# Kernel optimization log

Hardware: AMD Instinct MI355X
Metric: run time of the kernel (lower is better)

The kernel has to match this reference:

```python
import jax, jax.numpy as jnp
import numpy as np

H = 128
W = 128
DELTA = 7000.0  # sigmainv in the original (delta default 7000)


def setup_inputs() -> dict:
    key = jax.random.key(0)
    k1, k2, k3, k4 = jax.random.split(key, 4)
    B, P, F, TH, TW = 2, 300, 512, 512, 512
    points_bxpx3 = jax.random.uniform(k1, (B, P, 3), jnp.float32) * 2.0 - 1.0  # NDC cube [-1,1]
    faces_fx3 = jax.random.randint(k2, (F, 3), 0, P, dtype=jnp.int32)
    uv_bxpx2 = jax.random.uniform(k3, (B, P, 2), jnp.float32)  # texcoords in [0,1]
    texture_bx3xthxtw = jax.random.uniform(k4, (B, 3, TH, TW), jnp.float32)
    return {"points_bxpx3": points_bxpx3, "faces_fx3": faces_fx3,
            "uv_bxpx2": uv_bxpx2, "texture_bx3xthxtw": texture_bx3xthxtw}


def _edge(ax, ay, bx, by, px, py):
    # signed area * 2 of triangle (a, b, p); standard edge function
    return (bx - ax) * (py - ay) - (by - ay) * (px - ax)


def _seg_d2(ax, ay, bx, by, px, py):
    # squared distance from point p to segment (a, b)
    abx, aby = bx - ax, by - ay
    apx, apy = px - ax, py - ay
    denom = abx * abx + aby * aby + 1e-12
    t = jnp.clip((apx * abx + apy * aby) / denom, 0.0, 1.0)
    dx = apx - t * abx
    dy = apy - t * aby
    return dx * dx + dy * dy


def _rasterize(points_bxpx3, faces_fx3, feats_bxfx3xd, height, width, delta):
    """Soft DIB-R-style rasterizer.
    Returns (imfeat [B,H,W,D], improb [B,H,W,1]).
    """
    B = points_bxpx3.shape[0]
    v = points_bxpx3[:, faces_fx3]                      # (B,F,3,3) gathered face vertices
    x0, x1, x2 = (v[:, :, i, 0][:, :, None, None] for i in range(3))
    y0, y1, y2 = (v[:, :, i, 1][:, :, None, None] for i in range(3))
    z0, z1, z2 = (v[:, :, i, 2][:, :, None, None] for i in range(3))

    # pixel-center grid in NDC; y flipped (top row = +1)
    px = ((jnp.arange(width, dtype=points_bxpx3.dtype) + 0.5) / width * 2.0 - 1.0)[None, None, None, :]
    py = (1.0 - (jnp.arange(height, dtype=points_bxpx3.dtype) + 0.5) / height * 2.0)[None, None, :, None]

    area = _edge(x0, y0, x1, y1, x2, y2)                # (B,F,1,1) == normal_z (cross-product z)
    front = area > 1e-8                                  # front-facing (normalz > 0) cull
    inv_area = 1.0 / jnp.where(front, area, 1.0)

    w0 = _edge(x1, y1, x2, y2, px, py) * inv_area        # (B,F,H,W) barycentrics
    w1 = _edge(x2, y2, x0, y0, px, py) * inv_area
    w2 = _edge(x0, y0, x1, y1, px, py) * inv_area
    inside = front & (w0 >= 0) & (w1 >= 0) & (w2 >= 0)

    z_pix = w0 * z0 + w1 * z1 + w2 * z2                  # interpolated depth
    zbuf = jnp.where(inside, z_pix, -1e9)
    best = jnp.argmax(zbuf, axis=1)                      # (B,H,W) nearest covering face
    hit = jnp.any(inside, axis=1)[..., None].astype(points_bxpx3.dtype)  # (B,H,W,1)

    # gather winning barycentrics and per-face vertex features
    w = jnp.stack([w0, w1, w2], axis=-1)                 # (B,F,H,W,3)
    idx = jnp.broadcast_to(best[:, None, :, :, None], (B, 1, height, width, 3))
    wb = jnp.take_along_axis(w, idx, axis=1)[:, 0]       # (B,H,W,3)
    fb = jax.vmap(lambda f, i: f[i])(feats_bxfx3xd, best)  # (B,H,W,3,D)
    imfeat = jnp.einsum('bhwk,bhwkd->bhwd', wb, fb) * hit

    # soft coverage: prob of each face = exp(-delta * d2(pixel, triangle)); z-buffer blend
    d2 = jnp.minimum(
        jnp.minimum(_seg_d2(x0, y0, x1, y1, px, py), _seg_d2(x1, y1, x2, y2, px, py)),
        _seg_d2(x2, y2, x0, y0, px, py))
    d2 = jnp.where(inside, 0.0, d2)
    p = jnp.where(front, jnp.exp(-delta * d2), 0.0)      # (B,F,H,W)
    log_miss = jnp.sum(jnp.log1p(-jnp.clip(p, 0.0, 1.0 - 1e-7)), axis=1)  # (B,H,W)
    improb = (1.0 - jnp.exp(log_miss))[..., None]
    return imfeat, improb


def _fragmentshader(imtexcoords, texture_bx3xthxtw, hardmask):
    # bilinear texture sampling; background is zero
    B, C, TH, TW = texture_bx3xthxtw.shape
    u = jnp.clip(imtexcoords[..., 0], 0.0, 1.0)
    vv = jnp.clip(imtexcoords[..., 1], 0.0, 1.0)
    fx = u * (TW - 1)
    fy = (1.0 - vv) * (TH - 1)
    x0 = jnp.floor(fx).astype(jnp.int32); x1 = jnp.minimum(x0 + 1, TW - 1)
    y0 = jnp.floor(fy).astype(jnp.int32); y1 = jnp.minimum(y0 + 1, TH - 1)
    wx = (fx - x0)[:, None]; wy = (fy - y0)[:, None]     # (B,1,H,W)

    def g(tex, yy, xx):  # tex (C,TH,TW), yy/xx (H,W) -> (C,H,W)
        return tex[:, yy, xx]
    c00 = jax.vmap(g)(texture_bx3xthxtw, y0, x0)
    c01 = jax.vmap(g)(texture_bx3xthxtw, y0, x1)
    c10 = jax.vmap(g)(texture_bx3xthxtw, y1, x0)
    c11 = jax.vmap(g)(texture_bx3xthxtw, y1, x1)
    col = (c00 * (1 - wx) * (1 - wy) + c01 * wx * (1 - wy)
           + c10 * (1 - wx) * wy + c11 * wx * wy)        # (B,C,H,W)
    return col.transpose(0, 2, 3, 1) * hardmask          # (B,H,W,C)


def reference(points_bxpx3, faces_fx3, uv_bxpx2, texture_bx3xthxtw):
    # texture mode: per-face vertex features = [u, v, mask=1]
    uvf = uv_bxpx2[:, faces_fx3]                          # (B,F,3,2)
    ones = jnp.ones_like(uvf[..., :1])
    feats = jnp.concatenate([uvf, ones], axis=-1)         # (B,F,3,3)
    imfeat, improb = _rasterize(points_bxpx3, faces_fx3, feats, H, W, DELTA)
    imtexcoords = imfeat[..., :2]
    hardmask = jax.lax.stop_gradient(imfeat[..., 2:3])    # .detach() in the original
    imrender = _fragmentshader(imtexcoords, texture_bx3xthxtw, hardmask)
    return imrender, improb
```

## Files before the change

### kernel.cpp

```cpp
#include <hip/hip_runtime.h>
#include <math.h>

constexpr int kB = 2, kP = 300, kF = 512, kH = 128, kW = 128, kTH = 512, kTW = 512;
constexpr float kDelta = 7000.0f;
constexpr float kCut = 0.0363f;
constexpr float kThr2 = 0.012928f;
constexpr float kIntThr = 0.0785f;
constexpr float kLogInside = -15.9423847f;

__device__ __forceinline__ unsigned zmap(float f) {
    unsigned b = __float_as_uint(f);
    return (b & 0x80000000u) ? ~b : (b | 0x80000000u);
}

__global__ __launch_bounds__(512, 4) void render_all(const float* __restrict__ pts,
                                                     const int* __restrict__ faces,
                                                     const float* __restrict__ uvs,
                                                     const float* __restrict__ tex,
                                                     float* __restrict__ out) {
    __shared__ float4 sF[8][kF];
    __shared__ unsigned long long s_best[64];
    __shared__ float s_lm[64];
    __shared__ int s_wsum[8];
    float4* s_pxW = sF[0];
    int4* s_pxO = (int4*)(sF[0] + 64);

    int tile = (int)blockIdx.x;
    int b = tile >> 8;
    int rem = tile & 255;
    int ty = rem >> 4, tx = rem & 15;
    int tid = (int)threadIdx.x;
    int lane = tid & 63;
    int wv = tid >> 6;

    {
        int f = tid;
        int i0 = faces[f * 3 + 0], i1 = faces[f * 3 + 1], i2 = faces[f * 3 + 2];
        const float* pb = pts + b * kP * 3;
        float x0 = pb[i0 * 3], y0 = pb[i0 * 3 + 1], z0 = pb[i0 * 3 + 2];
        float x1 = pb[i1 * 3], y1 = pb[i1 * 3 + 1], z1 = pb[i1 * 3 + 2];
        float x2 = pb[i2 * 3], y2 = pb[i2 * 3 + 1], z2 = pb[i2 * 3 + 2];
        const float* ub = uvs + b * (kP * 2);
        float u0 = ub[i0 * 2], vv0 = ub[i0 * 2 + 1];
        float u1 = ub[i1 * 2], vv1 = ub[i1 * 2 + 1];
        float u2 = ub[i2 * 2], vv2 = ub[i2 * 2 + 1];
        float area = (x1 - x0) * (y2 - y0) - (y1 - y0) * (x2 - x0);
        bool front = area > 1e-8f;

        if (tid < 64) { s_best[tid] = 0ull; s_lm[tid] = 0.0f; }
        sF[0][f] = make_float4(0.0f, 0.0f, -1e30f, 0.0f);
        sF[1][f] = make_float4(0.0f, -1e30f, 0.0f, 0.0f);
        sF[2][f] = make_float4(-1e30f, 0.0f, 0.0f, 0.0f);
        unsigned long long bal = __ballot(front);
        if (lane == 0) s_wsum[wv] = __popcll(bal);
        __syncthreads();

        int base = 0;
#pragma unroll
        for (int w = 0; w < 8; ++w) base += (w < wv) ? s_wsum[w] : 0;
        int k = base + __popcll(bal & ((1ull << lane) - 1ull));

        if (front) {
            int slot = ((k & 7) << 6) | (k >> 3);
            float inv_a = 1.0f / area;
            float e0x = x2 - x1, e0y = y2 - y1;
            float e1x = x0 - x2, e1y = y0 - y2;
            float e2x = x1 - x0, e2y = y1 - y0;
            float l0 = fmaf(e0x, e0x, e0y * e0y);
            float l1 = fmaf(e1x, e1x, e1y * e1y);
            float l2 = fmaf(e2x, e2x, e2y * e2y);
            float s0 = rsqrtf(l0 + 1e-12f);
            float s1 = rsqrtf(l1 + 1e-12f);
            float s2 = rsqrtf(l2 + 1e-12f);
            float A0 = -e0y * s0, B0 = e0x * s0, C0 = (e0y * x1 - e0x * y1) * s0;
            float A1 = -e1y * s1, B1 = e1x * s1, C1 = (e1y * x2 - e1x * y2) * s1;
            float A2 = -e2y * s2, B2 = e2x * s2, C2 = (e2y * x0 - e2x * y0) * s2;
            float a0 = -e0y * inv_a, b0 = e0x * inv_a, c0 = (e0y * x1 - e0x * y1) * inv_a;
            float a1 = -e1y * inv_a, b1 = e1x * inv_a, c1 = (e1y * x2 - e1x * y2) * inv_a;
            float a2 = -e2y * inv_a, b2 = e2x * inv_a, c2 = (e2y * x0 - e2x * y0) * inv_a;
            sF[0][slot] = make_float4(A0, B0, C0, A1);
            sF[1][slot] = make_float4(B1, C1, A2, B2);
            sF[2][slot] = make_float4(C2,
                                      a0 * z0 + a1 * z1 + a2 * z2,
                                      b0 * z0 + b1 * z1 + b2 * z2,
                                      c0 * z0 + c1 * z1 + c2 * z2);
            sF[3][slot] = make_float4(e0x * s0, e0y * s0,
                                      -(e0x * x1 + e0y * y1) * s0, l0 * s0);
            sF[4][slot] = make_float4(e1x * s1, e1y * s1,
                                      -(e1x * x2 + e1y * y2) * s1, l1 * s1);
            sF[5][slot] = make_float4(e2x * s2, e2y * s2,
                                      -(e2x * x0 + e2y * y0) * s2, l2 * s2);
            sF[6][slot] = make_float4(a0 * u0 + a1 * u1 + a2 * u2,
                                      b0 * u0 + b1 * u1 + b2 * u2,
                                      c0 * u0 + c1 * u1 + c2 * u2, 0.0f);
            sF[7][slot] = make_float4(a0 * vv0 + a1 * vv1 + a2 * vv2,
                                      b0 * vv0 + b1 * vv1 + b2 * vv2,
                                      c0 * vv0 + c1 * vv1 + c2 * vv2, 0.0f);
        }
    }
    __syncthreads();

    int pyi = ty * 8 + (lane >> 3);
    int pxi = tx * 8 + (lane & 7);
    float px = ((float)pxi + 0.5f) * (2.0f / 128.0f) - 1.0f;
    float py = 1.0f - ((float)pyi + 0.5f) * (2.0f / 128.0f);

    float cx = (float)(tx * 8 + 4) * (2.0f / 128.0f) - 1.0f;
    float cy = 1.0f - (float)(ty * 8 + 4) * (2.0f / 128.0f);
    unsigned long long me, mi;
    {
        int slt = (wv << 6) + lane;
        float4 a4 = sF[0][slt];
        float4 b4 = sF[1][slt];
        float4 c4 = sF[2][slt];
        float4 t0 = sF[3][slt];
        float4 t1 = sF[4][slt];
        float4 t2 = sF[5][slt];
        float L0 = fmaf(a4.x, cx, fmaf(a4.y, cy, a4.z));
        float L1 = fmaf(a4.w, cx, fmaf(b4.x, cy, b4.y));
        float L2 = fmaf(b4.z, cx, fmaf(b4.w, cy, c4.x));
        float minc = fminf(fminf(L0, L1), L2);
        float s0 = fmaf(t0.x, cx, fmaf(t0.y, cy, t0.z));
        float s1 = fmaf(t1.x, cx, fmaf(t1.y, cy, t1.z));
        float s2 = fmaf(t2.x, cx, fmaf(t2.y, cy, t2.z));
        float q0 = L0 * L0, q1 = L1 * L1, q2 = L2 * L2;
        float c0 = (s0 >= 0.0f && s0 <= t0.w) ? q0 : 1e30f;
        float c1 = (s1 >= 0.0f && s1 <= t1.w) ? q1 : 1e30f;
        float c2 = (s2 >= 0.0f && s2 <= t2.w) ? q2 : 1e30f;
        float dv1 = fmaf(s0, s0, q0);
        float dv2 = fmaf(s1, s1, q1);
        float dv0 = fmaf(s2, s2, q2);
        float d2c = fminf(fminf(fminf(c0, c1), fminf(c2, dv0)), fminf(dv1, dv2));
        bool inter = minc >= kIntThr;
        bool admit = (minc >= 0.0f) | (d2c <= kThr2);
        mi = __ballot(inter);
        me = __ballot(admit && !inter);
    }

    float bestz = -1e9f;
    int besti = 1 << 30, icnt = 0;
    float lm = 0.0f;

    icnt += (int)__popcll(mi);
    while (mi) {
        int l = (int)__builtin_ctzll(mi);
        mi &= (mi - 1);
        int fs = (wv << 6) + l;
        int k = (l << 3) | wv;
        float4 h2 = sF[2][fs];
        float z = fmaf(h2.y, px, fmaf(h2.z, py, h2.w));
        if (z > bestz || (z == bestz && k < besti)) { bestz = z; besti = k; }
    }

    while (me) {
        int l = (int)__builtin_ctzll(me);
        me &= (me - 1);
        int fs = (wv << 6) + l;
        int k = (l << 3) | wv;
        float4 h0 = sF[0][fs];
        float4 h1 = sF[1][fs];
        float4 h2 = sF[2][fs];
        float4 t0 = sF[3][fs];
        float4 t1 = sF[4][fs];
        float4 t2 = sF[5][fs];
        float L0 = fmaf(h0.x, px, fmaf(h0.y, py, h0.z));
        float L1 = fmaf(h0.w, px, fmaf(h1.x, py, h1.y));
        float L2 = fmaf(h1.z, px, fmaf(h1.w, py, h2.x));
        float minL = fminf(fminf(L0, L1), L2);
        bool inside = minL >= 0.0f;
        float z = fmaf(h2.y, px, fmaf(h2.z, py, h2.w));
        if (inside && (z > bestz || (z == bestz && k < besti))) { bestz = z; besti = k; }
        icnt += inside ? 1 : 0;
        float s0 = fmaf(t0.x, px, fmaf(t0.y, py, t0.z));
        float s1 = fmaf(t1.x, px, fmaf(t1.y, py, t1.z));
        float s2 = fmaf(t2.x, px, fmaf(t2.y, py, t2.z));
        float q0 = L0 * L0, q1 = L1 * L1, q2 = L2 * L2;
        float c0 = (s0 >= 0.0f && s0 <= t0.w) ? q0 : 1e30f;
        float c1 = (s1 >= 0.0f && s1 <= t1.w) ? q1 : 1e30f;
        float c2 = (s2 >= 0.0f && s2 <= t2.w) ? q2 : 1e30f;
        float dv1 = fmaf(s0, s0, q0);
        float dv2 = fmaf(s1, s1, q1);
        float dv0 = fmaf(s2, s2, q2);
        float d2 = fminf(fminf(fminf(c0, c1), fminf(c2, dv0)), fminf(dv1, dv2));
        bool need = (!inside) & (fminf(fminf(fabsf(L0), fabsf(L1)), fabsf(L2)) < kCut);
        d2 = need ? d2 : 30.0f;
        float p = __expf(-kDelta * d2);
        p = fminf(p, 1.0f - 1e-7f);
        lm += __logf(1.0f - p);
    }
    lm = fmaf((float)icnt, kLogInside, lm);

    if (besti < (1 << 30)) {
        unsigned long long key = ((unsigned long long)zmap(bestz) << 32) |
                                 (unsigned long long)(511 - besti);
        atomicMax(&s_best[lane], key);
    }
    atomicAdd(&s_lm[lane], lm);
    __syncthreads();

    if (tid < 64) {
        unsigned long long key = s_best[tid];
        float improb = 1.0f - expf(s_lm[tid]);
        float u = 0.0f, v = 0.0f, mk = 0.0f;
        if (key != 0ull) {
            int bi = 511 - (int)(key & 0xFFFFFFFFull);
            int slot = ((bi & 7) << 6) | (bi >> 3);
            float4 uq = sF[6][slot];
            float4 vq = sF[7][slot];
            u = fmaf(uq.x, px, fmaf(uq.y, py, uq.z));
            v = fmaf(vq.x, px, fmaf(vq.y, py, vq.z));
            mk = 1.0f;
        }
        float uc = fminf(fmaxf(u, 0.0f), 1.0f);
        float vc = fminf(fmaxf(v, 0.0f), 1.0f);
        float fx = uc * (float)(kTW - 1);
        float fy = (1.0f - vc) * (float)(kTH - 1);
        int xi0 = (int)floorf(fx), yi0 = (int)floorf(fy);
        int xi1 = min(xi0 + 1, kTW - 1), yi1 = min(yi0 + 1, kTH - 1);
        float wx = fx - (float)xi0, wy = fy - (float)yi0;
        float w00 = (1.0f - wx) * (1.0f - wy) * mk;
        float w01 = wx * (1.0f - wy) * mk;
        float w10 = (1.0f - wx) * wy * mk;
        float w11 = wx * wy * mk;
        s_pxW[tid] = make_float4(w00, w01, w10, w11);
        s_pxO[tid] = make_int4(yi0 * kTW + xi0, yi0 * kTW + xi1,
                               yi1 * kTW + xi0, yi1 * kTW + xi1);
        out[kB * kH * kW * 3 + (b * kH + pyi) * kW + pxi] = improb;
    }
    __syncthreads();

    if (tid < 192) {
        int pix = tid & 63;
        int c = tid >> 6;
        float4 w = s_pxW[pix];
        int4 o = s_pxO[pix];
        const float* tc = tex + ((size_t)b * 3 + c) * kTH * kTW;
        float col = tc[o.x] * w.x + tc[o.y] * w.y + tc[o.z] * w.z + tc[o.w] * w.w;
        int qy = ty * 8 + (pix >> 3);
        int qx = tx * 8 + (pix & 7);
        out[((b * kH + qy) * kW + qx) * 3 + c] = col;
    }
}

extern "C" void kernel_launch(void* const* d_in, const int* in_sizes, int n_in,
                              void* d_out, int out_size, void* d_ws, size_t ws_size,
                              hipStream_t stream) {
    const float* pts = (const float*)d_in[0];
    const int* faces = (const int*)d_in[1];
    const float* uvs = (const float*)d_in[2];
    const float* tex = (const float*)d_in[3];
    float* out = (float*)d_out;
    render_all<<<kB * 256, 512, 0, stream>>>(pts, faces, uvs, tex, out);
}
```

Measured before the change: 17.26 us.

## Drop front-face compaction prefix sum and unroll face loops by two

Face setup no longer compacts front-facing faces through a ballot prefix sum and an extra block barrier. Each face now goes to a fixed slot, and back faces get sentinel edge values so they fail every test. The intersection and edge-candidate loops now handle two faces per iteration, so their shared-memory loads can be issued together for more instruction-level parallelism. The cost is more register pressure and a duplicate evaluation when the count is odd, which is masked by the 'two' flag. Because faces are no longer compacted, back faces can sit in slots that the later per-wave scan may still visit.

Result: slower. 17.62 us (+2.1%).

```diff
diff --git a/kernel.cpp b/kernel.cpp
--- a/kernel.cpp
+++ b/kernel.cpp
@@ -21,7 +21,6 @@
     __shared__ float4 sF[8][kF];
     __shared__ unsigned long long s_best[64];
     __shared__ float s_lm[64];
-    __shared__ int s_wsum[8];
     float4* s_pxW = sF[0];
     int4* s_pxO = (int4*)(sF[0] + 64);
 
@@ -48,55 +47,48 @@
         bool front = area > 1e-8f;
 
         if (tid < 64) { s_best[tid] = 0ull; s_lm[tid] = 0.0f; }
-        sF[0][f] = make_float4(0.0f, 0.0f, -1e30f, 0.0f);
-        sF[1][f] = make_float4(0.0f, -1e30f, 0.0f, 0.0f);
-        sF[2][f] = make_float4(-1e30f, 0.0f, 0.0f, 0.0f);
-        unsigned long long bal = __ballot(front);
-        if (lane == 0) s_wsum[wv] = __popcll(bal);
-        __syncthreads();
-
-        int base = 0;
-#pragma unroll
-        for (int w = 0; w < 8; ++w) base += (w < wv) ? s_wsum[w] : 0;
-        int k = base + __popcll(bal & ((1ull << lane) - 1ull));
-
+
+        int slot = ((f & 7) << 6) | (f >> 3);
+        float inv_a = front ? (1.0f / area) : 0.0f;
+        float e0x = x2 - x1, e0y = y2 - y1;
+        float e1x = x0 - x2, e1y = y0 - y2;
+        float e2x = x1 - x0, e2y = y1 - y0;
+        float l0 = fmaf(e0x, e0x, e0y * e0y);
+        float l1 = fmaf(e1x, e1x, e1y * e1y);
+        float l2 = fmaf(e2x, e2x, e2y * e2y);
+        float s0 = rsqrtf(l0 + 1e-12f);
+        float s1 = rsqrtf(l1 + 1e-12f);
+        float s2 = rsqrtf(l2 + 1e-12f);
+        float A0 = -e0y * s0, B0 = e0x * s0, C0 = (e0y * x1 - e0x * y1) * s0;
+        float A1 = -e1y * s1, B1 = e1x * s1, C1 = (e1y * x2 - e1x * y2) * s1;
+        float A2 = -e2y * s2, B2 = e2x * s2, C2 = (e2y * x0 - e2x * y0) * s2;
+        float a0 = -e0y * inv_a, b0 = e0x * inv_a, c0 = (e0y * x1 - e0x * y1) * inv_a;
+        float a1 = -e1y * inv_a, b1 = e1x * inv_a, c1 = (e1y * x2 - e1x * y2) * inv_a;
+        float a2 = -e2y * inv_a, b2 = e2x * inv_a, c2 = (e2y * x0 - e2x * y0) * inv_a;
         if (front) {
-            int slot = ((k & 7) << 6) | (k >> 3);
-            float inv_a = 1.0f / area;
-            float e0x = x2 - x1, e0y = y2 - y1;
-            float e1x = x0 - x2, e1y = y0 - y2;
-            float e2x = x1 - x0, e2y = y1 - y0;
-            float l0 = fmaf(e0x, e0x, e0y * e0y);
-            float l1 = fmaf(e1x, e1x, e1y * e1y);
-            float l2 = fmaf(e2x, e2x, e2y * e2y);
-            float s0 = rsqrtf(l0 + 1e-12f);
-            float s1 = rsqrtf(l1 + 1e-12f);
-            float s2 = rsqrtf(l2 + 1e-12f);
-            float A0 = -e0y * s0, B0 = e0x * s0, C0 = (e0y * x1 - e0x * y1) * s0;
-            float A1 = -e1y * s1, B1 = e1x * s1, C1 = (e1y * x2 - e1x * y2) * s1;
-            float A2 = -e2y * s2, B2 = e2x * s2, C2 = (e2y * x0 - e2x * y0) * s2;
-            float a0 = -e0y * inv_a, b0 = e0x * inv_a, c0 = (e0y * x1 - e0x * y1) * inv_a;
-            float a1 = -e1y * inv_a, b1 = e1x * inv_a, c1 = (e1y * x2 - e1x * y2) * inv_a;
-            float a2 = -e2y * inv_a, b2 = e2x * inv_a, c2 = (e2y * x0 - e2x * y0) * inv_a;
             sF[0][slot] = make_float4(A0, B0, C0, A1);
             sF[1][slot] = make_float4(B1, C1, A2, B2);
             sF[2][slot] = make_float4(C2,
                                       a0 * z0 + a1 * z1 + a2 * z2,
                                       b0 * z0 + b1 * z1 + b2 * z2,
                                       c0 * z0 + c1 * z1 + c2 * z2);
-            sF[3][slot] = make_float4(e0x * s0, e0y * s0,
-                                      -(e0x * x1 + e0y * y1) * s0, l0 * s0);
-            sF[4][slot] = make_float4(e1x * s1, e1y * s1,
-                                      -(e1x * x2 + e1y * y2) * s1, l1 * s1);
-            sF[5][slot] = make_float4(e2x * s2, e2y * s2,
-                                      -(e2x * x0 + e2y * y0) * s2, l2 * s2);
-            sF[6][slot] = make_float4(a0 * u0 + a1 * u1 + a2 * u2,
-                                      b0 * u0 + b1 * u1 + b2 * u2,
-                                      c0 * u0 + c1 * u1 + c2 * u2, 0.0f);
-            sF[7][slot] = make_float4(a0 * vv0 + a1 * vv1 + a2 * vv2,
-                                      b0 * vv0 + b1 * vv1 + b2 * vv2,
-                                      c0 * vv0 + c1 * vv1 + c2 * vv2, 0.0f);
-        }
+        } else {
+            sF[0][slot] = make_float4(0.0f, 0.0f, -1e30f, 0.0f);
+            sF[1][slot] = make_float4(0.0f, -1e30f, 0.0f, 0.0f);
+            sF[2][slot] = make_float4(-1e30f, 0.0f, 0.0f, 0.0f);
+        }
+        sF[3][slot] = make_float4(e0x * s0, e0y * s0,
+                                  -(e0x * x1 + e0y * y1) * s0, l0 * s0);
+        sF[4][slot] = make_float4(e1x * s1, e1y * s1,
+                                  -(e1x * x2 + e1y * y2) * s1, l1 * s1);
+        sF[5][slot] = make_float4(e2x * s2, e2y * s2,
+                                  -(e2x * x0 + e2y * y0) * s2, l2 * s2);
+        sF[6][slot] = make_float4(a0 * u0 + a1 * u1 + a2 * u2,
+                                  b0 * u0 + b1 * u1 + b2 * u2,
+                                  c0 * u0 + c1 * u1 + c2 * u2, 0.0f);
+        sF[7][slot] = make_float4(a0 * vv0 + a1 * vv1 + a2 * vv2,
+                                  b0 * vv0 + b1 * vv1 + b2 * vv2,
+                                  c0 * vv0 + c1 * vv1 + c2 * vv2, 0.0f);
     }
     __syncthreads();
 
@@ -145,48 +137,77 @@
     while (mi) {
         int l = (int)__builtin_ctzll(mi);
         mi &= (mi - 1);
-        int fs = (wv << 6) + l;
-        int k = (l << 3) | wv;
-        float4 h2 = sF[2][fs];
-        float z = fmaf(h2.y, px, fmaf(h2.z, py, h2.w));
-        if (z > bestz || (z == bestz && k < besti)) { bestz = z; besti = k; }
+        bool two = mi != 0;
+        int l2 = two ? (int)__builtin_ctzll(mi) : l;
+        if (two) mi &= (mi - 1);
+        float4 hA = sF[2][(wv << 6) + l];
+        float4 hB = sF[2][(wv << 6) + l2];
+        int kA = (l << 3) | wv, kB = (l2 << 3) | wv;
+        float zA = fmaf(hA.y, px, fmaf(hA.z, py, hA.w));
+        float zB = fmaf(hB.y, px, fmaf(hB.z, py, hB.w));
+        if (zA > bestz || (zA == bestz && kA < besti)) { bestz = zA; besti = kA; }
+        if (zB > bestz || (zB == bestz && kB < besti)) { bestz = zB; besti = kB; }
     }
 
     while (me) {
-        int l = (int)__builtin_ctzll(me);
+        int la = (int)__builtin_ctzll(me);
         me &= (me - 1);
-        int fs = (wv << 6) + l;
-        int k = (l << 3) | wv;
-        float4 h0 = sF[0][fs];
-        float4 h1 = sF[1][fs];
-        float4 h2 = sF[2][fs];
-        float4 t0 = sF[3][fs];
-        float4 t1 = sF[4][fs];
-        float4 t2 = sF[5][fs];
-        float L0 = fmaf(h0.x, px, fmaf(h0.y, py, h0.z));
-        float L1 = fmaf(h0.w, px, fmaf(h1.x, py, h1.y));
-        float L2 = fmaf(h1.z, px, fmaf(h1.w, py, h2.x));
-        float minL = fminf(fminf(L0, L1), L2);
-        bool inside = minL >= 0.0f;
-        float z = fmaf(h2.y, px, fmaf(h2.z, py, h2.w));
-        if (inside && (z > bestz || (z == bestz && k < besti))) { bestz = z; besti = k; }
-        icnt += inside ? 1 : 0;
-        float s0 = fmaf(t0.x, px, fmaf(t0.y, py, t0.z));
-        float s1 = fmaf(t1.x, px, fmaf(t1.y, py, t1.z));
-        float s2 = fmaf(t2.x, px, fmaf(t2.y, py, t2.z));
-        float q0 = L0 * L0, q1 = L1 * L1, q2 = L2 * L2;
-        float c0 = (s0 >= 0.0f && s0 <= t0.w) ? q0 : 1e30f;
-        float c1 = (s1 >= 0.0f && s1 <= t1.w) ? q1 : 1e30f;
-        float c2 = (s2 >= 0.0f && s2 <= t2.w) ? q2 : 1e30f;
-        float dv1 = fmaf(s0, s0, q0);
-        float dv2 = fmaf(s1, s1, q1);
-        float dv0 = fmaf(s2, s2, q2);
-        float d2 = fminf(fminf(fminf(c0, c1), fminf(c2, dv0)), fminf(dv1, dv2));
-        bool need = (!inside) & (fminf(fminf(fabsf(L0), fabsf(L1)), fabsf(L2)) < kCut);
-        d2 = need ? d2 : 30.0f;
-        float p = __expf(-kDelta * d2);
-        p = fminf(p, 1.0f - 1e-7f);
-        lm += __logf(1.0f - p);
+        bool two = me != 0;
+        int lb = two ? (int)__builtin_ctzll(me) : la;
+        if (two) me &= (me - 1);
+        int fsa = (wv << 6) + la, fsb = (wv << 6) + lb;
+        int ka = (la << 3) | wv, kb = (lb << 3) | wv;
+        float4 Ah0 = sF[0][fsa], Ah1 = sF[1][fsa], Ah2 = sF[2][fsa];
+        float4 At0 = sF[3][fsa], At1 = sF[4][fsa], At2 = sF[5][fsa];
+        float4 Bh0 = sF[0][fsb], Bh1 = sF[1][fsb], Bh2 = sF[2][fsb];
+        float4 Bt0 = sF[3][fsb], Bt1 = sF[4][fsb], Bt2 = sF[5][fsb];
+
+        {
+            float L0 = fmaf(Ah0.x, px, fmaf(Ah0.y, py, Ah0.z));
+            float L1 = fmaf(Ah0.w, px, fmaf(Ah1.x, py, Ah1.y));
+            float L2 = fmaf(Ah1.z, px, fmaf(Ah1.w, py, Ah2.x));
+            bool inside = fminf(fminf(L0, L1), L2) >= 0.0f;
+            float z = fmaf(Ah2.y, px, fmaf(Ah2.z, py, Ah2.w));
+            if (inside && (z > bestz || (z == bestz && ka < besti))) { bestz = z; besti = ka; }
+            icnt += inside ? 1 : 0;
+            float s0 = fmaf(At0.x, px, fmaf(At0.y, py, At0.z));
+            float s1 = fmaf(At1.x, px, fmaf(At1.y, py, At1.z));
+            float s2 = fmaf(At2.x, px, fmaf(At2.y, py, At2.z));
+            float q0 = L0 * L0, q1 = L1 * L1, q2 = L2 * L2;
+            float c0 = (s0 >= 0.0f && s0 <= At0.w) ? q0 : 1e30f;
+            float c1 = (s1 >= 0.0f && s1 <= At1.w) ? q1 : 1e30f;
+            float c2 = (s2 >= 0.0f && s2 <= At2.w) ? q2 : 1e30f;
+            float d2 = fminf(fminf(fminf(c0, c1), fminf(c2, fmaf(s2, s2, q2))),
+                             fminf(fmaf(s0, s0, q0), fmaf(s1, s1, q1)));
+            bool need = (!inside) &
+                        (fminf(fminf(fabsf(L0), fabsf(L1)), fabsf(L2)) < kCut);
+            d2 = need ? d2 : 30.0f;
+            float p = fminf(__expf(-kDelta * d2), 1.0f - 1e-7f);
+            lm += __logf(1.0f - p);
+        }
+        {
+            float L0 = fmaf(Bh0.x, px, fmaf(Bh0.y, py, Bh0.z));
+            float L1 = fmaf(Bh0.w, px, fmaf(Bh1.x, py, Bh1.y));
+            float L2 = fmaf(Bh1.z, px, fmaf(Bh1.w, py, Bh2.x));
+            bool inside = (fminf(fminf(L0, L1), L2) >= 0.0f) && two;
+            float z = fmaf(Bh2.y, px, fmaf(Bh2.z, py, Bh2.w));
+            if (inside && (z > bestz || (z == bestz && kb < besti))) { bestz = z; besti = kb; }
+            icnt += inside ? 1 : 0;
+            float s0 = fmaf(Bt0.x, px, fmaf(Bt0.y, py, Bt0.z));
+            float s1 = fmaf(Bt1.x, px, fmaf(Bt1.y, py, Bt1.z));
+            float s2 = fmaf(Bt2.x, px, fmaf(Bt2.y, py, Bt2.z));
+            float q0 = L0 * L0, q1 = L1 * L1, q2 = L2 * L2;
+            float c0 = (s0 >= 0.0f && s0 <= Bt0.w) ? q0 : 1e30f;
+            float c1 = (s1 >= 0.0f && s1 <= Bt1.w) ? q1 : 1e30f;
+            float c2 = (s2 >= 0.0f && s2 <= Bt2.w) ? q2 : 1e30f;
+            float d2 = fminf(fminf(fminf(c0, c1), fminf(c2, fmaf(s2, s2, q2))),
+                             fminf(fmaf(s0, s0, q0), fmaf(s1, s1, q1)));
+            bool need = (!inside) && two &&
+                        (fminf(fminf(fabsf(L0), fabsf(L1)), fabsf(L2)) < kCut);
+            d2 = need ? d2 : 30.0f;
+            float p = fminf(__expf(-kDelta * d2), 1.0f - 1e-7f);
+            lm += __logf(1.0f - p);
+        }
     }
     lm = fmaf((float)icnt, kLogInside, lm);
 
```
